# Optimization experiments

Measured on AMD Instinct MI355X. Metric: run time of the kernel, lower is better.

## Reference

```python
import jax, jax.numpy as jnp
import numpy as np

N = 50000       # nodes
E_RAND = 800000 # random edges (avg degree ~16)
K = 64          # edges touching `node`; setup_inputs guarantees exactly K
F = 64          # num_node_features
C = 64          # conv_channels


def setup_inputs() -> dict:
    key = jax.random.key(0)
    ks = jax.random.split(key, 6)
    x = jax.random.normal(ks[0], (N, F), dtype=jnp.float32)
    # random edges avoiding node 0 so exactly the K prepended edges touch node 0
    src = jax.random.randint(ks[1], (E_RAND,), 1, N, dtype=jnp.int64)
    dst = jax.random.randint(ks[2], (E_RAND,), 1, N, dtype=jnp.int64)
    ksrc = jnp.zeros((K,), dtype=jnp.int64)
    kdst = jnp.arange(1, K + 1, dtype=jnp.int64)
    edge_index = jnp.stack([jnp.concatenate([ksrc, src]),
                            jnp.concatenate([kdst, dst])])  # [2, K+E_RAND]
    W1 = jax.random.normal(ks[3], (F, C), jnp.float32) / np.float32(np.sqrt(F))
    b1 = jnp.zeros((C,), jnp.float32)
    W2 = jax.random.normal(ks[4], (C, C), jnp.float32) / np.float32(np.sqrt(C))
    b2 = jnp.zeros((C,), jnp.float32)
    Wr = jax.random.normal(ks[5], (C, 1), jnp.float32) / np.float32(np.sqrt(C))
    br = jnp.zeros((1,), jnp.float32)
    return {"x": x, "edge_index": edge_index, "node": 0,
            "W1": W1, "b1": b1, "W2": W2, "b2": b2, "Wr": Wr, "br": br}


def gcn_conv(x, src, dst, W, b):
    """PyG GCNConv with self-loops already appended to (src, dst).
    out[v] = sum_{(u,v)} deg(u)^-1/2 * deg(v)^-1/2 * (x @ W)[u] + b
    """
    n = x.shape[0]
    xw = x @ W                                              # [N, C]
    deg = jnp.zeros((n,), xw.dtype).at[dst].add(1.0)        # in-degree incl. self-loop
    dinv = jnp.where(deg > 0, jax.lax.rsqrt(deg), 0.0)
    norm = dinv[src] * dinv[dst]                            # [E]
    out = jax.ops.segment_sum(xw[src] * norm[:, None], dst, num_segments=n)
    return out + b


def reference(x, edge_index, node, W1, b1, W2, b2, Wr, br):
    n = x.shape[0]
    loop = jnp.arange(n, dtype=edge_index.dtype)
    src = jnp.concatenate([edge_index[0], loop])  # add self loops (GCNConv default)
    dst = jnp.concatenate([edge_index[1], loop])
    h = jax.nn.relu(gcn_conv(x, src, dst, W1, b1))
    h = jax.nn.relu(gcn_conv(h, src, dst, W2, b2))
    # edges incident to `node` (setup guarantees exactly K such edges)
    s0, d0 = edge_index[0], edge_index[1]
    mask = (s0 == node) | (d0 == node)
    idx = jnp.nonzero(mask, size=K)[0]
    s, d = s0[idx], d0[idx]
    targets = jnp.where(s == node, d, s)  # self-loop (s==d==node) -> node
    score = h[targets] @ Wr + br          # [K, 1]
    score = jax.nn.softmax(score, axis=0)
    return score[:, 0], targets
```

## Files before the change

### kernel.cpp

```cpp
#include <hip/hip_runtime.h>
#include <math.h>

#define KK 64
#define CAP 64
#define NF 4160

__global__ __launch_bounds__(256) void k_count(const int* __restrict__ ei, int E,
                                               const int* __restrict__ nodep,
                                               int* __restrict__ cnt,
                                               int* __restrict__ tcount,
                                               int* __restrict__ tpairs) {
    int node = nodep[0];
    int n4 = E >> 2;
    int e4 = blockIdx.x * 256 + threadIdx.x;
    if (e4 < n4) {
        int4 ss = ((const int4*)ei)[e4];
        int4 dd = ((const int4*)(ei + E))[e4];
        int s[4] = {ss.x, ss.y, ss.z, ss.w};
        int d[4] = {dd.x, dd.y, dd.z, dd.w};
#pragma unroll
        for (int k = 0; k < 4; k++) {
            atomicAdd(&cnt[d[k]], 1);
            if (s[k] == node || d[k] == node) {
                int q = atomicAdd(tcount, 1);
                if (q < KK) { int e = e4 * 4 + k; tpairs[2 * q] = e; tpairs[2 * q + 1] = (s[k] == node) ? d[k] : s[k]; }
            }
        }
    }
    if (blockIdx.x == 0 && threadIdx.x == 0) {
        for (int e = n4 * 4; e < E; e++) {
            int s = ei[e], d = ei[E + e];
            atomicAdd(&cnt[d], 1);
            if (s == node || d == node) {
                int q = atomicAdd(tcount, 1);
                if (q < KK) { tpairs[2 * q] = e; tpairs[2 * q + 1] = (s == node) ? d : s; }
            }
        }
    }
}

__global__ void k_tsort(const int* __restrict__ tpairs, int* __restrict__ tsorted,
                        int* __restrict__ towner, int* __restrict__ tflag,
                        float* __restrict__ h1s) {
    __shared__ int eidx[KK], tgt[KK], srt[KK];
    int t = threadIdx.x;
    h1s[(size_t)NF * 64 + t] = 0.f;
    eidx[t] = tpairs[2 * t];
    tgt[t] = tpairs[2 * t + 1];
    __syncthreads();
    int rank = 0;
    for (int j = 0; j < KK; j++) rank += (eidx[j] < eidx[t]) ? 1 : 0;
    srt[rank] = tgt[t];
    __syncthreads();
    int mynode = srt[t];
    int owner = t;
    for (int j = 0; j < t; j++) if (srt[j] == mynode) { owner = j; break; }
    tsorted[t] = mynode;
    towner[t] = owner;
    if (owner == t) tflag[mynode] = t + 1;
}

__global__ __launch_bounds__(256) void k_collect_t(const int* __restrict__ ei, int E,
                                                   const int* __restrict__ tflag,
                                                   int* __restrict__ tcnt2,
                                                   int* __restrict__ tslots) {
    int n4 = E >> 2;
    int e4 = blockIdx.x * 256 + threadIdx.x;
    if (e4 < n4) {
        int4 ss = ((const int4*)ei)[e4];
        int4 dd = ((const int4*)(ei + E))[e4];
        int s[4] = {ss.x, ss.y, ss.z, ss.w};
        int d[4] = {dd.x, dd.y, dd.z, dd.w};
#pragma unroll
        for (int k = 0; k < 4; k++) {
            int f = tflag[d[k]];
            if (f) { int p = atomicAdd(&tcnt2[f - 1], 1); if (p < CAP) tslots[(f - 1) * CAP + p] = s[k]; }
        }
    }
    if (blockIdx.x == 0 && threadIdx.x == 0) {
        for (int e = n4 * 4; e < E; e++) {
            int f = tflag[ei[E + e]];
            if (f) { int p = atomicAdd(&tcnt2[f - 1], 1); if (p < CAP) tslots[(f - 1) * CAP + p] = ei[e]; }
        }
    }
}

__global__ __launch_bounds__(1024) void k_fbuild(const int* __restrict__ tsorted,
                                                 const int* __restrict__ towner,
                                                 const int* __restrict__ tcnt2,
                                                 const int* __restrict__ tslots,
                                                 int* __restrict__ fnode,
                                                 int* __restrict__ fmapRow,
                                                 int* __restrict__ fidx) {
    int tid = threadIdx.x;
    for (int i = tid; i < NF; i += 1024) {
        int tp = i / 65, j = i % 65;
        int own = towner[tp];
        int u;
        if (j == 0) u = tsorted[tp];
        else {
            int c = tcnt2[own]; if (c > CAP) c = CAP;
            u = (j - 1 < c) ? tslots[own * CAP + (j - 1)] : -1;
        }
        fnode[i] = u;
    }
    __syncthreads();
    for (int i = tid; i < NF; i += 1024) {
        int u = fnode[i];
        if (u >= 0) atomicCAS(&fmapRow[u], 0, i + 1);
    }
    __syncthreads();
    for (int i = tid; i < NF; i += 1024) {
        int u = fnode[i];
        fidx[i] = (u >= 0) ? (fmapRow[u] - 1) : NF;
    }
}

__global__ __launch_bounds__(256) void k_collect_f(const int* __restrict__ ei, int E,
                                                   const int* __restrict__ fmapRow,
                                                   int* __restrict__ fcnt,
                                                   int* __restrict__ fslots) {
    int n4 = E >> 2;
    int e4 = blockIdx.x * 256 + threadIdx.x;
    if (e4 < n4) {
        int4 ss = ((const int4*)ei)[e4];
        int4 dd = ((const int4*)(ei + E))[e4];
        int s[4] = {ss.x, ss.y, ss.z, ss.w};
        int d[4] = {dd.x, dd.y, dd.z, dd.w};
#pragma unroll
        for (int k = 0; k < 4; k++) {
            int r = fmapRow[d[k]];
            if (r) { int p = atomicAdd(&fcnt[r - 1], 1); if (p < CAP) fslots[(size_t)(r - 1) * CAP + p] = s[k]; }
        }
    }
    if (blockIdx.x == 0 && threadIdx.x == 0) {
        for (int e = n4 * 4; e < E; e++) {
            int r = fmapRow[ei[E + e]];
            if (r) { int p = atomicAdd(&fcnt[r - 1], 1); if (p < CAP) fslots[(size_t)(r - 1) * CAP + p] = ei[e]; }
        }
    }
}

__global__ __launch_bounds__(256) void k_layer1(const float* __restrict__ x,
                                                const int* __restrict__ fnode,
                                                const int* __restrict__ fmapRow,
                                                const int* __restrict__ cnt,
                                                const int* __restrict__ fcnt,
                                                const int* __restrict__ fslots,
                                                const float* __restrict__ W1,
                                                const float* __restrict__ b1,
                                                float* __restrict__ h1s) {
    __shared__ __align__(16) float W1s[64 * 64];
    int tid = threadIdx.x;
    for (int i = tid; i < 1024; i += 256) ((float4*)W1s)[i] = ((const float4*)W1)[i];
    __syncthreads();
    int i = blockIdx.x * 4 + (tid >> 6);
    int lane = tid & 63;
    if (i >= NF) return;
    int u = fnode[i];
    if (u < 0 || fmapRow[u] != i + 1) return;
    float du = rsqrtf((float)(cnt[u] + 1));
    float acc = du * x[(size_t)u * 64 + lane];
    int c = fcnt[i]; if (c > CAP) c = CAP;
    const int* sl = fslots + (size_t)i * CAP;
    int k = 0;
    for (; k + 4 <= c; k += 4) {
        int u0 = sl[k], u1 = sl[k + 1], u2 = sl[k + 2], u3 = sl[k + 3];
        float f0 = rsqrtf((float)(cnt[u0] + 1));
        float f1 = rsqrtf((float)(cnt[u1] + 1));
        float f2 = rsqrtf((float)(cnt[u2] + 1));
        float f3 = rsqrtf((float)(cnt[u3] + 1));
        acc += f0 * x[(size_t)u0 * 64 + lane] + f1 * x[(size_t)u1 * 64 + lane]
             + f2 * x[(size_t)u2 * 64 + lane] + f3 * x[(size_t)u3 * 64 + lane];
    }
    for (; k < c; k++) {
        int uu = sl[k];
        acc += rsqrtf((float)(cnt[uu] + 1)) * x[(size_t)uu * 64 + lane];
    }
    float z = du * acc;
    float h = 0.f;
#pragma unroll
    for (int f = 0; f < 64; f++) h += __shfl(z, f) * W1s[f * 64 + lane];
    h = fmaxf(h + b1[lane], 0.f);
    h1s[(size_t)i * 64 + lane] = du * h;
}

__global__ __launch_bounds__(64) void k_score2(const float* __restrict__ h1s,
                                               const int* __restrict__ fidx,
                                               const int* __restrict__ tsorted,
                                               const int* __restrict__ cnt,
                                               const float* __restrict__ W2,
                                               const float* __restrict__ b2,
                                               const float* __restrict__ Wr,
                                               float* __restrict__ sc) {
    int tp = blockIdx.x;
    int lane = threadIdx.x;
    int t = tsorted[tp];
    float dt = rsqrtf((float)(cnt[t] + 1));
    const int* fx = fidx + tp * 65;
    float z = 0.f;
#pragma unroll
    for (int j = 0; j < 65; j++) {
        int idx = fx[j];
        z += h1s[(size_t)idx * 64 + lane];
    }
    z *= dt;
    float acc = 0.f;
#pragma unroll
    for (int f = 0; f < 64; f++) acc += __shfl(z, f) * W2[f * 64 + lane];
    float h2 = fmaxf(acc + b2[lane], 0.f);
    float p = h2 * Wr[lane];
#pragma unroll
    for (int off = 32; off >= 1; off >>= 1) p += __shfl_xor(p, off);
    if (lane == 0) sc[tp] = p;
}

__global__ void k_softmax(const float* __restrict__ sc, const int* __restrict__ tsorted,
                          float* __restrict__ out) {
    int t = threadIdx.x;
    float s = sc[t];
    float m = s;
#pragma unroll
    for (int off = 32; off >= 1; off >>= 1) m = fmaxf(m, __shfl_xor(m, off));
    float e = __expf(s - m);
    float ss = e;
#pragma unroll
    for (int off = 32; off >= 1; off >>= 1) ss += __shfl_xor(ss, off);
    out[t] = e / ss;
    out[KK + t] = (float)tsorted[t];
}

extern "C" void kernel_launch(void* const* d_in, const int* in_sizes, int n_in,
                              void* d_out, int out_size, void* d_ws, size_t ws_size,
                              hipStream_t stream) {
    const float* x  = (const float*)d_in[0];
    const int*   ei = (const int*)d_in[1];
    const int*   nodep = (const int*)d_in[2];
    const float* W1 = (const float*)d_in[3];
    const float* b1 = (const float*)d_in[4];
    const float* W2 = (const float*)d_in[5];
    const float* b2 = (const float*)d_in[6];
    const float* Wr = (const float*)d_in[7];
    const float* br = (const float*)d_in[8];
    float* out = (float*)d_out;
    (void)br;

    int N = in_sizes[0] / 64;
    int E = in_sizes[1] / 2;

    char* w = (char*)d_ws;
    int* cnt     = (int*)w; w += (size_t)N * 4;
    int* tflag   = (int*)w; w += (size_t)N * 4;
    int* fmapRow = (int*)w; w += (size_t)N * 4;
    int* fcnt    = (int*)w; w += (size_t)NF * 4;
    int* tcnt2   = (int*)w; w += KK * 4;
    int* tcount  = (int*)w; w += 16;
    size_t zbytes = (size_t)(3 * N + NF + KK) * 4 + 16;
    int* tpairs  = (int*)w; w += 2 * KK * 4;
    int* tsorted = (int*)w; w += KK * 4;
    int* towner  = (int*)w; w += KK * 4;
    int* fnode   = (int*)w; w += (size_t)NF * 4;
    int* fidx    = (int*)w; w += (size_t)NF * 4;
    int* tslots  = (int*)w; w += (size_t)KK * CAP * 4;
    int* fslots  = (int*)w; w += (size_t)NF * CAP * 4;
    float* h1s   = (float*)w; w += (size_t)(NF + 1) * 64 * 4;
    float* sc    = (float*)w; w += KK * 4;

    hipMemsetAsync(cnt, 0, zbytes, stream);

    int ebl = (E / 4 + 255) / 256;
    k_count<<<ebl, 256, 0, stream>>>(ei, E, nodep, cnt, tcount, tpairs);
    k_tsort<<<1, 64, 0, stream>>>(tpairs, tsorted, towner, tflag, h1s);
    k_collect_t<<<ebl, 256, 0, stream>>>(ei, E, tflag, tcnt2, tslots);
    k_fbuild<<<1, 1024, 0, stream>>>(tsorted, towner, tcnt2, tslots, fnode, fmapRow, fidx);
    k_collect_f<<<ebl, 256, 0, stream>>>(ei, E, fmapRow, fcnt, fslots);
    k_layer1<<<(NF + 3) / 4, 256, 0, stream>>>(x, fnode, fmapRow, cnt, fcnt, fslots, W1, b1, h1s);
    k_score2<<<KK, 64, 0, stream>>>(h1s, fidx, tsorted, cnt, W2, b2, Wr, sc);
    k_softmax<<<1, 64, 0, stream>>>(sc, tsorted, out);
}
```

Baseline: 173.2 us.

## Fold workspace zeroing into find kernel and merge degree count with target collection

The big workspace memset is replaced by zeroing inside the first edge-scan kernel, with only the small counter still cleared by a memset. Degree counting moves out of the first scan and into the second scan, which also collects target neighbors, so the first scan only looks for edges touching the node. The aim is to drop one memset pass and rebalance work across the edge passes. Correctness depends on the grid covering the whole zero region (zcount4 int4s must fit within ebl*256 threads) and on all zeroed fields being used only in later kernels.

```diff
diff --git a/kernel.cpp b/kernel.cpp
--- a/kernel.cpp
+++ b/kernel.cpp
@@ -5,12 +5,65 @@
 #define CAP 64
 #define NF 4160
 
-__global__ __launch_bounds__(256) void k_count(const int* __restrict__ ei, int E,
-                                               const int* __restrict__ nodep,
-                                               int* __restrict__ cnt,
-                                               int* __restrict__ tcount,
-                                               int* __restrict__ tpairs) {
+__global__ __launch_bounds__(256) void k_find(const int* __restrict__ ei, int E,
+                                              const int* __restrict__ nodep,
+                                              int4* __restrict__ zbase, int zcount4,
+                                              float* __restrict__ h1s,
+                                              int* __restrict__ tcount,
+                                              int* __restrict__ tpairs) {
+    int idx = blockIdx.x * 256 + threadIdx.x;
+    if (idx < zcount4) zbase[idx] = make_int4(0, 0, 0, 0);
+    if (idx < 64) h1s[(size_t)NF * 64 + idx] = 0.f;
     int node = nodep[0];
+    int n4 = E >> 2;
+    if (idx < n4) {
+        int4 ss = ((const int4*)ei)[idx];
+        int4 dd = ((const int4*)(ei + E))[idx];
+        int s[4] = {ss.x, ss.y, ss.z, ss.w};
+        int d[4] = {dd.x, dd.y, dd.z, dd.w};
+#pragma unroll
+        for (int k = 0; k < 4; k++) {
+            if (s[k] == node || d[k] == node) {
+                int q = atomicAdd(tcount, 1);
+                if (q < KK) { int e = idx * 4 + k; tpairs[2 * q] = e; tpairs[2 * q + 1] = (s[k] == node) ? d[k] : s[k]; }
+            }
+        }
+    }
+    if (idx == 0) {
+        for (int e = n4 * 4; e < E; e++) {
+            int s = ei[e], d = ei[E + e];
+            if (s == node || d == node) {
+                int q = atomicAdd(tcount, 1);
+                if (q < KK) { tpairs[2 * q] = e; tpairs[2 * q + 1] = (s == node) ? d : s; }
+            }
+        }
+    }
+}
+
+__global__ void k_tsort(const int* __restrict__ tpairs, int* __restrict__ tsorted,
+                        int* __restrict__ towner, int* __restrict__ tflag) {
+    __shared__ int eidx[KK], tgt[KK], srt[KK];
+    int t = threadIdx.x;
+    eidx[t] = tpairs[2 * t];
+    tgt[t] = tpairs[2 * t + 1];
+    __syncthreads();
+    int rank = 0;
+    for (int j = 0; j < KK; j++) rank += (eidx[j] < eidx[t]) ? 1 : 0;
+    srt[rank] = tgt[t];
+    __syncthreads();
+    int mynode = srt[t];
+    int owner = t;
+    for (int j = 0; j < t; j++) if (srt[j] == mynode) { owner = j; break; }
+    tsorted[t] = mynode;
+    towner[t] = owner;
+    if (owner == t) tflag[mynode] = t + 1;
+}
+
+__global__ __launch_bounds__(256) void k_cct(const int* __restrict__ ei, int E,
+                                             const int* __restrict__ tflag,
+                                             int* __restrict__ cnt,
+                                             int* __restrict__ tcnt2,
+                                             int* __restrict__ tslots) {
     int n4 = E >> 2;
     int e4 = blockIdx.x * 256 + threadIdx.x;
     if (e4 < n4) {
@@ -21,65 +74,15 @@
 #pragma unroll
         for (int k = 0; k < 4; k++) {
             atomicAdd(&cnt[d[k]], 1);
-            if (s[k] == node || d[k] == node) {
-                int q = atomicAdd(tcount, 1);
-                if (q < KK) { int e = e4 * 4 + k; tpairs[2 * q] = e; tpairs[2 * q + 1] = (s[k] == node) ? d[k] : s[k]; }
-            }
+            int f = tflag[d[k]];
+            if (f) { int p = atomicAdd(&tcnt2[f - 1], 1); if (p < CAP) tslots[(f - 1) * CAP + p] = s[k]; }
         }
     }
     if (blockIdx.x == 0 && threadIdx.x == 0) {
         for (int e = n4 * 4; e < E; e++) {
-            int s = ei[e], d = ei[E + e];
+            int d = ei[E + e];
             atomicAdd(&cnt[d], 1);
-            if (s == node || d == node) {
-                int q = atomicAdd(tcount, 1);
-                if (q < KK) { tpairs[2 * q] = e; tpairs[2 * q + 1] = (s == node) ? d : s; }
-            }
-        }
-    }
-}
-
-__global__ void k_tsort(const int* __restrict__ tpairs, int* __restrict__ tsorted,
-                        int* __restrict__ towner, int* __restrict__ tflag,
-                        float* __restrict__ h1s) {
-    __shared__ int eidx[KK], tgt[KK], srt[KK];
-    int t = threadIdx.x;
-    h1s[(size_t)NF * 64 + t] = 0.f;
-    eidx[t] = tpairs[2 * t];
-    tgt[t] = tpairs[2 * t + 1];
-    __syncthreads();
-    int rank = 0;
-    for (int j = 0; j < KK; j++) rank += (eidx[j] < eidx[t]) ? 1 : 0;
-    srt[rank] = tgt[t];
-    __syncthreads();
-    int mynode = srt[t];
-    int owner = t;
-    for (int j = 0; j < t; j++) if (srt[j] == mynode) { owner = j; break; }
-    tsorted[t] = mynode;
-    towner[t] = owner;
-    if (owner == t) tflag[mynode] = t + 1;
-}
-
-__global__ __launch_bounds__(256) void k_collect_t(const int* __restrict__ ei, int E,
-                                                   const int* __restrict__ tflag,
-                                                   int* __restrict__ tcnt2,
-                                                   int* __restrict__ tslots) {
-    int n4 = E >> 2;
-    int e4 = blockIdx.x * 256 + threadIdx.x;
-    if (e4 < n4) {
-        int4 ss = ((const int4*)ei)[e4];
-        int4 dd = ((const int4*)(ei + E))[e4];
-        int s[4] = {ss.x, ss.y, ss.z, ss.w};
-        int d[4] = {dd.x, dd.y, dd.z, dd.w};
-#pragma unroll
-        for (int k = 0; k < 4; k++) {
-            int f = tflag[d[k]];
-            if (f) { int p = atomicAdd(&tcnt2[f - 1], 1); if (p < CAP) tslots[(f - 1) * CAP + p] = s[k]; }
-        }
-    }
-    if (blockIdx.x == 0 && threadIdx.x == 0) {
-        for (int e = n4 * 4; e < E; e++) {
-            int f = tflag[ei[E + e]];
+            int f = tflag[d];
             if (f) { int p = atomicAdd(&tcnt2[f - 1], 1); if (p < CAP) tslots[(f - 1) * CAP + p] = ei[e]; }
         }
     }
@@ -254,8 +257,8 @@
     int* fmapRow = (int*)w; w += (size_t)N * 4;
     int* fcnt    = (int*)w; w += (size_t)NF * 4;
     int* tcnt2   = (int*)w; w += KK * 4;
+    int zcount4 = (3 * N + NF + KK) / 4;
     int* tcount  = (int*)w; w += 16;
-    size_t zbytes = (size_t)(3 * N + NF + KK) * 4 + 16;
     int* tpairs  = (int*)w; w += 2 * KK * 4;
     int* tsorted = (int*)w; w += KK * 4;
     int* towner  = (int*)w; w += KK * 4;
@@ -266,12 +269,12 @@
     float* h1s   = (float*)w; w += (size_t)(NF + 1) * 64 * 4;
     float* sc    = (float*)w; w += KK * 4;
 
-    hipMemsetAsync(cnt, 0, zbytes, stream);
+    hipMemsetAsync(tcount, 0, 16, stream);
 
     int ebl = (E / 4 + 255) / 256;
-    k_count<<<ebl, 256, 0, stream>>>(ei, E, nodep, cnt, tcount, tpairs);
-    k_tsort<<<1, 64, 0, stream>>>(tpairs, tsorted, towner, tflag, h1s);
-    k_collect_t<<<ebl, 256, 0, stream>>>(ei, E, tflag, tcnt2, tslots);
+    k_find<<<ebl, 256, 0, stream>>>(ei, E, nodep, (int4*)cnt, zcount4, h1s, tcount, tpairs);
+    k_tsort<<<1, 64, 0, stream>>>(tpairs, tsorted, towner, tflag);
+    k_cct<<<ebl, 256, 0, stream>>>(ei, E, tflag, cnt, tcnt2, tslots);
     k_fbuild<<<1, 1024, 0, stream>>>(tsorted, towner, tcnt2, tslots, fnode, fmapRow, fidx);
     k_collect_f<<<ebl, 256, 0, stream>>>(ei, E, fmapRow, fcnt, fslots);
     k_layer1<<<(NF + 3) / 4, 256, 0, stream>>>(x, fnode, fmapRow, cnt, fcnt, fslots, W1, b1, h1s);
```

Measured after the change: 171.5 us. Within noise of the previous version (-1.0%).
